# Performance work log

Hardware: AMD Instinct MI355X
Metric: run time of the kernel (lower is better)

The kernel has to match this reference:

```python
import jax, jax.numpy as jnp
import numpy as np

N_NODES = 20000
N_EDGES = 160000
F_IN = 256
N_CLASSES = 32
HEADS = 8
GAT_C = 128


def setup_inputs() -> dict:
    key = jax.random.key(0)
    ks = jax.random.split(key, 20)

    def w(k, shape, fan_in):
        return jax.random.normal(k, shape, dtype=jnp.float32) * (1.0 / np.sqrt(fan_in))

    return {
        "x": jax.random.normal(ks[0], (N_NODES, F_IN), dtype=jnp.float32),
        "edge_index": jax.random.randint(ks[1], (2, N_EDGES), 0, N_NODES, dtype=jnp.int64),
        # SAGEConv(256 -> 64): lin_l (bias) on aggregated neighbors, lin_r (no bias) on root
        "W_l1": w(ks[2], (F_IN, 64), F_IN), "b_l1": jnp.zeros((64,), jnp.float32),
        "W_r1": w(ks[3], (F_IN, 64), F_IN),
        # SAGEConv(64 -> 128)
        "W_l2": w(ks[4], (64, 128), 64), "b_l2": jnp.zeros((128,), jnp.float32),
        "W_r2": w(ks[5], (64, 128), 64),
        # GATConv(128 -> 128, heads=8, concat)
        "W_g": w(ks[6], (128, HEADS * GAT_C), 128),
        "att_src": w(ks[7], (HEADS, GAT_C), GAT_C),
        "att_dst": w(ks[8], (HEADS, GAT_C), GAT_C),
        "b_g": jnp.zeros((HEADS * GAT_C,), jnp.float32),
        # GCNConv(1024 -> 64), GCNConv(64 -> 32)
        "W_c1": w(ks[9], (HEADS * GAT_C, 64), HEADS * GAT_C), "b_c1": jnp.zeros((64,), jnp.float32),
        "W_c2": w(ks[10], (64, N_CLASSES), 64), "b_c2": jnp.zeros((N_CLASSES,), jnp.float32),
        # residual Linear(256 -> 64)
        "W_res": w(ks[11], (F_IN, 64), F_IN), "b_res": jnp.zeros((64,), jnp.float32),
    }


def _forward(x, edge_index, W_l1, b_l1, W_r1, W_l2, b_l2, W_r2,
             W_g, att_src, att_dst, b_g, W_c1, b_c1, W_c2, b_c2, W_res, b_res):
    n = x.shape[0]
    src, dst = edge_index[0], edge_index[1]  # messages flow src -> dst

    def sage(h, Wl, bl, Wr):
        # mean aggregation of neighbor features, then lin_l(agg) + lin_r(root)
        s = jax.ops.segment_sum(h[src], dst, num_segments=n)
        cnt = jax.ops.segment_sum(jnp.ones_like(src, dtype=h.dtype), dst, num_segments=n)
        mean = s / jnp.maximum(cnt, 1.0)[:, None]
        return mean @ Wl + bl + h @ Wr

    res_x = x @ W_res + b_res
    h = jax.nn.relu(sage(x, W_l1, b_l1, W_r1)) + res_x      # [N, 64]
    h = jax.nn.relu(sage(h, W_l2, b_l2, W_r2))              # [N, 128]

    # ---- GATConv with self-loops (PyG default) ----
    loop = jnp.arange(n, dtype=src.dtype)
    srcf = jnp.concatenate([src, loop])
    dstf = jnp.concatenate([dst, loop])

    hg = (h @ W_g).reshape(n, HEADS, GAT_C)                 # [N, H, C]
    a_s = jnp.sum(hg * att_src, axis=-1)                    # [N, H]
    a_d = jnp.sum(hg * att_dst, axis=-1)                    # [N, H]
    e = jax.nn.leaky_relu(a_s[srcf] + a_d[dstf], negative_slope=0.2)  # [Ef, H]
    m = jax.ops.segment_max(e, dstf, num_segments=n)
    e = jnp.exp(e - m[dstf])
    denom = jax.ops.segment_sum(e, dstf, num_segments=n)
    alpha = e / denom[dstf]                                 # softmax over incoming edges
    gat = jax.ops.segment_sum(alpha[:, :, None] * hg[srcf], dstf, num_segments=n)
    h = jax.nn.relu(gat.reshape(n, HEADS * GAT_C) + b_g)    # [N, 1024]

    # ---- GCNConv with self-loops and symmetric normalization ----
    deg = jax.ops.segment_sum(jnp.ones_like(srcf, dtype=h.dtype), dstf, num_segments=n)
    dinv = jax.lax.rsqrt(jnp.maximum(deg, 1.0))             # deg >= 1 via self-loops
    norm = (dinv[srcf] * dinv[dstf])[:, None]

    def gcn(h, W, b):
        hw = h @ W
        return jax.ops.segment_sum(norm * hw[srcf], dstf, num_segments=n) + b

    h = gcn(h, W_c1, b_c1)
    h = gcn(h, W_c2, b_c2)
    return jax.nn.log_softmax(h, axis=1)


def reference(x, edge_index, W_l1, b_l1, W_r1, W_l2, b_l2, W_r2,
              W_g, att_src, att_dst, b_g, W_c1, b_c1, W_c2, b_c2, W_res, b_res):
    return _forward(x, edge_index, W_l1, b_l1, W_r1, W_l2, b_l2, W_r2,
                    W_g, att_src, att_dst, b_g, W_c1, b_c1, W_c2, b_c2, W_res, b_res)
```

## Files before the change

kernel.cpp:

```cpp
#include <hip/hip_runtime.h>

#define NN 20000
#define NE 160000
#define NEF 180000
#define NB1 ((NN + 255) / 256)

typedef long long ll;
typedef __attribute__((ext_vector_type(4))) float f32x4;
typedef __attribute__((ext_vector_type(8))) short s16x8;

static __device__ __forceinline__ float b2f(ushort u) {
  return __uint_as_float(((unsigned)u) << 16);
}
static __device__ __forceinline__ ushort f2b(float f) {
  unsigned u = __float_as_uint(f);
  return (ushort)((u + 0x7fffu + ((u >> 16) & 1u)) >> 16);
}

template<int MF, int NF, int K, bool F32OUT>
__global__ __launch_bounds__(256) void gemm_mfma(
    const ushort* __restrict__ A, const ushort* __restrict__ Bt,
    const float* __restrict__ bias, void* __restrict__ Cv,
    int M, int N, int lda)
{
  const int wid  = threadIdx.x >> 6;
  const int lane = threadIdx.x & 63;
  const int wr = wid >> 1, wc = wid & 1;
  const int bm = blockIdx.y * (32 * MF) + wr * (16 * MF);
  const int bn = blockIdx.x * (32 * NF) + wc * (16 * NF);
  const int lr = lane & 15;
  const int ko = (lane >> 4) * 8;

  const ushort* pa[MF];
  const ushort* pb[NF];
  #pragma unroll
  for (int i = 0; i < MF; i++) {
    int r = min(bm + i * 16 + lr, M - 1);
    pa[i] = A + (ll)r * lda + ko;
  }
  #pragma unroll
  for (int j = 0; j < NF; j++) {
    int c = min(bn + j * 16 + lr, N - 1);
    pb[j] = Bt + (ll)c * K + ko;
  }

  f32x4 acc[MF][NF];
  #pragma unroll
  for (int i = 0; i < MF; i++)
    #pragma unroll
    for (int j = 0; j < NF; j++) acc[i][j] = {0.f, 0.f, 0.f, 0.f};

  #pragma unroll
  for (int k = 0; k < K; k += 32) {
    s16x8 af[MF], bf[NF];
    #pragma unroll
    for (int i = 0; i < MF; i++) af[i] = *(const s16x8*)(pa[i] + k);
    #pragma unroll
    for (int j = 0; j < NF; j++) bf[j] = *(const s16x8*)(pb[j] + k);
    #pragma unroll
    for (int i = 0; i < MF; i++)
      #pragma unroll
      for (int j = 0; j < NF; j++)
        acc[i][j] = __builtin_amdgcn_mfma_f32_16x16x32_bf16(af[i], bf[j], acc[i][j], 0, 0, 0);
  }

  const int rq = (lane >> 4) * 4;
  #pragma unroll
  for (int i = 0; i < MF; i++) {
    #pragma unroll
    for (int j = 0; j < NF; j++) {
      int col = bn + j * 16 + lr;
      if (col >= N) continue;
      float bv = bias ? bias[col] : 0.f;
      int rbase = bm + i * 16 + rq;
      #pragma unroll
      for (int r = 0; r < 4; r++) {
        int row = rbase + r;
        if (row >= M) continue;
        float v = acc[i][j][r] + bv;
        if (F32OUT) ((float*)Cv)[(ll)row * N + col] = v;
        else        ((ushort*)Cv)[(ll)row * N + col] = f2b(v);
      }
    }
  }
}

__global__ __launch_bounds__(256) void k_gat_apply_gcn1(
    const ushort* __restrict__ agg,
    const ushort* __restrict__ BtG,
    const ushort* __restrict__ Btc1,
    const float* __restrict__ b_g,
    ushort* __restrict__ hw64)
{
  __shared__ ushort gt[2][32][72];
  const int wc   = threadIdx.x >> 6;
  const int lane = threadIdx.x & 63;
  const int bm = blockIdx.x * 32;
  const int lr = lane & 15;
  const int ko = (lane >> 4) * 8;
  const int rq = (lane >> 4) * 4;

  const ushort* pa0 = agg + (ll)min(bm + lr,      NN - 1) * 1024 + ko;
  const ushort* pa1 = agg + (ll)min(bm + 16 + lr, NN - 1) * 1024 + ko;

  f32x4 o0 = {0.f, 0.f, 0.f, 0.f}, o1 = o0;

  #pragma unroll 2
  for (int ct = 0; ct < 16; ct++) {
    const int koff = (ct >> 1) * 128;
    const int cg = ct * 64 + wc * 16 + lr;
    const ushort* pb = BtG + (ll)cg * 128 + ko;
    f32x4 g0 = {0.f, 0.f, 0.f, 0.f}, g1 = g0;
    #pragma unroll
    for (int k = 0; k < 128; k += 32) {
      s16x8 a0 = *(const s16x8*)(pa0 + koff + k);
      s16x8 a1 = *(const s16x8*)(pa1 + koff + k);
      s16x8 bb = *(const s16x8*)(pb + k);
      g0 = __builtin_amdgcn_mfma_f32_16x16x32_bf16(a0, bb, g0, 0, 0, 0);
      g1 = __builtin_amdgcn_mfma_f32_16x16x32_bf16(a1, bb, g1, 0, 0, 0);
    }
    float bv = b_g[cg];
    #pragma unroll
    for (int r = 0; r < 4; r++) {
      gt[ct & 1][rq + r][wc * 16 + lr]      = f2b(fmaxf(g0[r] + bv, 0.f));
      gt[ct & 1][16 + rq + r][wc * 16 + lr] = f2b(fmaxf(g1[r] + bv, 0.f));
    }
    __syncthreads();
    const ushort* qb = Btc1 + (ll)(wc * 16 + lr) * 1024 + ct * 64 + ko;
    #pragma unroll
    for (int k = 0; k < 64; k += 32) {
      s16x8 a0 = *(const s16x8*)&gt[ct & 1][lr][k + ko];
      s16x8 a1 = *(const s16x8*)&gt[ct & 1][16 + lr][k + ko];
      s16x8 bb = *(const s16x8*)(qb + k);
      o0 = __builtin_amdgcn_mfma_f32_16x16x32_bf16(a0, bb, o0, 0, 0, 0);
      o1 = __builtin_amdgcn_mfma_f32_16x16x32_bf16(a1, bb, o1, 0, 0, 0);
    }
  }
  int col = wc * 16 + lr;
  #pragma unroll
  for (int r = 0; r < 4; r++) {
    int row0 = bm + rq + r, row1 = bm + 16 + rq + r;
    if (row0 < NN) hw64[(ll)row0 * 64 + col] = f2b(o0[r]);
    if (row1 < NN) hw64[(ll)row1 * 64 + col] = f2b(o1[r]);
  }
}

struct PrepEnt { const float* W; ushort* Bt; int N; int K; int base; };
struct Prep { PrepEnt e[8]; int total; };

__global__ void k_setup(const float* __restrict__ x, ushort* __restrict__ xb, Prep p,
                        const float* __restrict__ b_res, const float* __restrict__ b_l1,
                        const float* __restrict__ b_l2, float* __restrict__ bias192,
                        float* __restrict__ bias256,
                        const float* __restrict__ W_g, const float* __restrict__ att_s,
                        const float* __restrict__ att_d, ushort* __restrict__ watt_t,
                        int* __restrict__ icnt) {
  ll t = (ll)blockIdx.x * 256 + threadIdx.x;
  const ll T0 = (ll)NN * 64;
  if (t < T0) {
    ll i = t * 4;
    float4 v = *(const float4*)(x + i);
    ushort4 o;
    o.x = f2b(v.x); o.y = f2b(v.y); o.z = f2b(v.z); o.w = f2b(v.w);
    *(ushort4*)(xb + i) = o;
    return;
  }
  t -= T0;
  if (t < p.total) {
    int tt = (int)t;
    #pragma unroll
    for (int i = 0; i < 8; i++) {
      int sz = p.e[i].N * p.e[i].K;
      if (tt >= p.e[i].base && tt < p.e[i].base + sz) {
        int loc = tt - p.e[i].base;
        int n = loc / p.e[i].K, k = loc - n * p.e[i].K;
        p.e[i].Bt[loc] = f2b(p.e[i].W[(ll)k * p.e[i].N + n]);
      }
    }
    return;
  }
  t -= p.total;
  if (t < 256) {
    int tt = (int)t;
    if (tt < 64) bias192[tt] = b_res[tt];
    else if (tt < 128) bias192[tt] = 0.f;
    else if (tt < 192) bias192[tt] = b_l1[tt - 128];
    bias256[tt] = (tt < 128) ? 0.f : b_l2[tt - 128];
    return;
  }
  t -= 256;
  if (t < 2048) {
    int k = (int)t >> 4;
    int col = (int)t & 15;
    int h = col & 7;
    const float* av = (col < 8) ? (att_s + h * 128) : (att_d + h * 128);
    const float* wrow = W_g + (ll)k * 1024 + h * 128;
    float s = 0.f;
    for (int j = 0; j < 128; j++) s += wrow[j] * av[j];
    watt_t[col * 128 + k] = f2b(s);
    return;
  }
  t -= 2048;
  if (t < NN) icnt[t] = 0;
}

__global__ void k_counti(const int* __restrict__ dst, int* __restrict__ icnt) {
  int e = blockIdx.x * 256 + threadIdx.x;
  if (e < NE) atomicAdd(&icnt[dst[e]], 1);
}

__global__ __launch_bounds__(256) void k_scan1(const int* __restrict__ icnt,
                                               int* __restrict__ rowptr,
                                               int* __restrict__ bsum) {
  __shared__ int sd[256];
  int t = threadIdx.x;
  int i = blockIdx.x * 256 + t;
  int v = (i < NN) ? icnt[i] + 1 : 0;
  sd[t] = v;
  __syncthreads();
  #pragma unroll
  for (int o = 1; o < 256; o <<= 1) {
    int u = (t >= o) ? sd[t - o] : 0;
    __syncthreads();
    sd[t] += u;
    __syncthreads();
  }
  if (i < NN) rowptr[i] = sd[t] - v;
  if (t == 255) bsum[blockIdx.x] = sd[255];
}

__global__ __launch_bounds__(128) void k_scan2(const int* __restrict__ bsum,
                                               int* __restrict__ boff) {
  __shared__ int sd[128];
  int t = threadIdx.x;
  int v = (t < NB1) ? bsum[t] : 0;
  sd[t] = v;
  __syncthreads();
  #pragma unroll
  for (int o = 1; o < 128; o <<= 1) {
    int u = (t >= o) ? sd[t - o] : 0;
    __syncthreads();
    sd[t] += u;
    __syncthreads();
  }
  if (t < NB1) boff[t] = sd[t] - v;
}

__global__ void k_scan3(int* __restrict__ rowptr, const int* __restrict__ boff,
                        int* __restrict__ cur, const int* __restrict__ icnt,
                        float* __restrict__ dinv) {
  int i = blockIdx.x * 256 + threadIdx.x;
  if (i >= NN) return;
  int r = rowptr[i] + boff[i >> 8];
  rowptr[i] = r;
  cur[i] = r;
  dinv[i] = rsqrtf((float)icnt[i] + 1.0f);
  if (i == 0) rowptr[NN] = NEF;
}

__global__ void k_scatter(const int* __restrict__ dst, int* __restrict__ cur,
                          int* __restrict__ eid) {
  int t = blockIdx.x * 256 + threadIdx.x;
  if (t >= NEF) return;
  int d = (t < NE) ? dst[t] : t - NE;
  int p = atomicAdd(&cur[d], 1);
  eid[p] = t;
}

template<int C, int STRIDE, bool ADD_RES>
__global__ __launch_bounds__(256) void k_sage_csr(
    const int* __restrict__ rowptr, const int* __restrict__ eid,
    const int* __restrict__ src, const ushort* __restrict__ feat,
    const ushort* __restrict__ linr, const ushort* __restrict__ resx,
    ushort* __restrict__ out)
{
  int node = blockIdx.x * 4 + (threadIdx.x >> 6);
  int lane = threadIdx.x & 63;
  if (node >= NN) return;
  int b = rowptr[node], e = rowptr[node + 1];
  float a0 = 0.f, a1 = 0.f;
  int n = 0;
  for (int base = b; base < e; base += 64) {
    int m = min(64, e - base);
    int sreg = -1;
    if (lane < m) {
      int ed = eid[base + lane];
      sreg = (ed < NE) ? src[ed] : -1;
    }
    for (int i = 0; i < m; i++) {
      int s = __shfl(sreg, i);
      if (s >= 0) {
        a0 += b2f(feat[(ll)s * STRIDE + lane]);
        if (C == 128) a1 += b2f(feat[(ll)s * STRIDE + lane + 64]);
        n++;
      }
    }
  }
  float inv = 1.f / fmaxf((float)n, 1.f);
  {
    float v = a0 * inv + b2f(linr[(ll)node * STRIDE + lane]);
    v = fmaxf(v, 0.f);
    if (ADD_RES) v += b2f(resx[(ll)node * STRIDE + lane]);
    out[(ll)node * C + lane] = f2b(v);
  }
  if (C == 128) {
    float v = a1 * inv + b2f(linr[(ll)node * STRIDE + lane + 64]);
    v = fmaxf(v, 0.f);
    out[(ll)node * C + lane + 64] = f2b(v);
  }
}

__global__ void k_gat_softmax(const int* __restrict__ rowptr, const int* __restrict__ eid,
                              const int* __restrict__ src, const float* __restrict__ asd,
                              float* __restrict__ alpha, float* __restrict__ invden) {
  int t = blockIdx.x * 256 + threadIdx.x;
  if (t >= NN * 8) return;
  int node = t >> 3, h = t & 7;
  int b = rowptr[node], e = rowptr[node + 1];
  float ad = asd[(ll)node * 16 + 8 + h];
  float mx = -3.0e38f;
  for (int p = b; p < e; p++) {
    int ed = eid[p];
    int s = (ed < NE) ? src[ed] : node;
    float v = asd[(ll)s * 16 + h] + ad;
    v = (v > 0.f) ? v : 0.2f * v;
    mx = fmaxf(mx, v);
  }
  float sum = 0.f;
  for (int p = b; p < e; p++) {
    int ed = eid[p];
    int s = (ed < NE) ? src[ed] : node;
    float v = asd[(ll)s * 16 + h] + ad;
    v = (v > 0.f) ? v : 0.2f * v;
    float ex = expf(v - mx);
    alpha[(ll)p * 8 + h] = ex;
    sum += ex;
  }
  invden[t] = 1.f / sum;
}

__global__ __launch_bounds__(128) void k_gat_agg(
    const int* __restrict__ rowptr, const int* __restrict__ eid,
    const int* __restrict__ src, const float* __restrict__ alpha,
    const float* __restrict__ invden, const ushort* __restrict__ h2b,
    ushort* __restrict__ agg)
{
  __shared__ int s_l[64];
  __shared__ float al[64 * 8];
  __shared__ float inv_s[8];
  int node = blockIdx.x;
  int c = threadIdx.x;
  int b = rowptr[node], e = rowptr[node + 1];
  if (c < 8) inv_s[c] = invden[node * 8 + c];
  float acc[8] = {0.f, 0.f, 0.f, 0.f, 0.f, 0.f, 0.f, 0.f};
  for (int c0 = b; c0 < e; c0 += 64) {
    int m = min(64, e - c0);
    if (c < m) { int ed = eid[c0 + c]; s_l[c] = (ed < NE) ? src[ed] : node; }
    for (int idx = c; idx < m * 8; idx += 128) al[idx] = alpha[(ll)c0 * 8 + idx];
    __syncthreads();
    for (int i = 0; i < m; i++) {
      float v = b2f(h2b[(ll)s_l[i] * 128 + c]);
      float4 aa = *(const float4*)&al[i * 8];
      float4 ab = *(const float4*)&al[i * 8 + 4];
      acc[0] = fmaf(aa.x, v, acc[0]);
      acc[1] = fmaf(aa.y, v, acc[1]);
      acc[2] = fmaf(aa.z, v, acc[2]);
      acc[3] = fmaf(aa.w, v, acc[3]);
      acc[4] = fmaf(ab.x, v, acc[4]);
      acc[5] = fmaf(ab.y, v, acc[5]);
      acc[6] = fmaf(ab.z, v, acc[6]);
      acc[7] = fmaf(ab.w, v, acc[7]);
    }
    __syncthreads();
  }
  #pragma unroll
  for (int h = 0; h < 8; h++)
    agg[(ll)node * 1024 + h * 128 + c] = f2b(acc[h] * inv_s[h]);
}

template<int C, bool FUSE_LSM>
__global__ __launch_bounds__(256) void k_gcn_csr(
    const int* __restrict__ rowptr, const int* __restrict__ eid,
    const int* __restrict__ src, const float* __restrict__ dinv,
    const ushort* __restrict__ hw, const float* __restrict__ bias,
    void* __restrict__ outv)
{
  const int npb = 256 / C;
  int node = blockIdx.x * npb + threadIdx.x / C;
  int c = threadIdx.x & (C - 1);
  if (node >= NN) return;
  int b = rowptr[node], e = rowptr[node + 1];
  float acc = 0.f;
  for (int base = b; base < e; base += C) {
    int m = min(C, e - base);
    int sreg = 0;
    float dreg = 0.f;
    if (c < m) {
      int ed = eid[base + c];
      sreg = (ed < NE) ? src[ed] : node;
      dreg = dinv[sreg];
    }
    for (int i = 0; i < m; i++) {
      int s  = __shfl(sreg, i, C);
      float dv = __shfl(dreg, i, C);
      acc = fmaf(dv, b2f(hw[(ll)s * C + c]), acc);
    }
  }
  float v = acc * dinv[node] + bias[c];
  if (!FUSE_LSM) {
    ((ushort*)outv)[(ll)node * C + c] = f2b(v);
  } else {
    float mx = v;
    #pragma unroll
    for (int o = 16; o > 0; o >>= 1) mx = fmaxf(mx, __shfl_xor(mx, o, 32));
    float s = expf(v - mx);
    #pragma unroll
    for (int o = 16; o > 0; o >>= 1) s += __shfl_xor(s, o, 32);
    ((float*)outv)[(ll)node * C + c] = v - mx - logf(s);
  }
}

extern "C" void kernel_launch(void* const* d_in, const int* in_sizes, int n_in,
                              void* d_out, int out_size, void* d_ws, size_t ws_size,
                              hipStream_t stream) {
  const float* x     = (const float*)d_in[0];
  const int*   ei    = (const int*)d_in[1];
  const float* W_l1  = (const float*)d_in[2];
  const float* b_l1  = (const float*)d_in[3];
  const float* W_r1  = (const float*)d_in[4];
  const float* W_l2  = (const float*)d_in[5];
  const float* b_l2  = (const float*)d_in[6];
  const float* W_r2  = (const float*)d_in[7];
  const float* W_g   = (const float*)d_in[8];
  const float* att_s = (const float*)d_in[9];
  const float* att_d = (const float*)d_in[10];
  const float* b_g   = (const float*)d_in[11];
  const float* W_c1  = (const float*)d_in[12];
  const float* b_c1  = (const float*)d_in[13];
  const float* W_c2  = (const float*)d_in[14];
  const float* b_c2  = (const float*)d_in[15];
  const float* W_res = (const float*)d_in[16];
  const float* b_res = (const float*)d_in[17];
  const int* src = ei;
  const int* dst = ei + NE;
  float* out = (float*)d_out;

  float* Wf = (float*)d_ws;
  size_t off = 0;
  auto take = [&](size_t n) { float* p = Wf + off; off += (n + 3) & ~(size_t)3; return p; };
  ushort* xb    = (ushort*)take((size_t)NN * 128);
  ushort* C192  = (ushort*)take((size_t)NN * 96);
  ushort* h1    = (ushort*)take((size_t)NN * 32);
  ushort* C256  = (ushort*)take((size_t)NN * 128);
  ushort* h2    = (ushort*)take((size_t)NN * 64);
  ushort* agg   = (ushort*)take((size_t)NN * 512);
  ushort* hw64  = (ushort*)take((size_t)NN * 32);
  ushort* acc64 = (ushort*)take((size_t)NN * 32);
  ushort* hw32  = (ushort*)take((size_t)NN * 16);
  ushort* Bt192 = (ushort*)take(192 * 256 / 2);
  ushort* Bt256 = (ushort*)take(256 * 64 / 2);
  ushort* BtG   = (ushort*)take(1024 * 128 / 2);
  ushort* Btc1  = (ushort*)take(64 * 1024 / 2);
  ushort* Btc2  = (ushort*)take(32 * 64 / 2);
  ushort* watt_t= (ushort*)take(16 * 128 / 2);
  float* bias192 = take(192);
  float* bias256 = take(256);
  int*   icnt   = (int*)take(NN);
  int*   rowptr = (int*)take(NN + 1);
  int*   cur    = (int*)take(NN);
  int*   eidb   = (int*)take(NEF);
  int*   bsum   = (int*)take(NB1);
  int*   boff   = (int*)take(NB1);
  float* dinv   = take(NN);
  float* asd    = take((size_t)NN * 16);
  float* alpha  = take((size_t)NEF * 8);
  float* invden = take((size_t)NN * 8);
  (void)ws_size; (void)in_sizes; (void)n_in; (void)out_size;

  auto nb = [](ll t) { return dim3((unsigned)((t + 255) / 256)); };

  Prep pp;
  int base = 0;
  auto ent = [&](int i, const float* W, ushort* Bt, int N_, int K_) {
    pp.e[i] = {W, Bt, N_, K_, base}; base += N_ * K_;
  };
  ent(0, W_res, Bt192,             64, 256);
  ent(1, W_l1,  Bt192 + 64 * 256,  64, 256);
  ent(2, W_r1,  Bt192 + 128 * 256, 64, 256);
  ent(3, W_l2,  Bt256,             128, 64);
  ent(4, W_r2,  Bt256 + 128 * 64,  128, 64);
  ent(5, W_g,   BtG,               1024, 128);
  ent(6, W_c1,  Btc1,              64, 1024);
  ent(7, W_c2,  Btc2,              32, 64);
  pp.total = base;
  k_setup<<<nb((ll)NN * 64 + base + 256 + 2048 + NN), 256, 0, stream>>>(
      x, xb, pp, b_res, b_l1, b_l2, bias192, bias256, W_g, att_s, att_d, watt_t, icnt);

  k_counti<<<nb(NE), 256, 0, stream>>>(dst, icnt);
  k_scan1<<<NB1, 256, 0, stream>>>(icnt, rowptr, bsum);
  k_scan2<<<1, 128, 0, stream>>>(bsum, boff);
  k_scan3<<<nb(NN), 256, 0, stream>>>(rowptr, boff, cur, icnt, dinv);
  k_scatter<<<nb(NEF), 256, 0, stream>>>(dst, cur, eidb);

  gemm_mfma<4, 2, 256, false><<<dim3(3, 157), 256, 0, stream>>>(
      xb, Bt192, bias192, C192, NN, 192, 256);
  k_sage_csr<64, 192, true><<<nb((ll)NN * 64), 256, 0, stream>>>(
      rowptr, eidb, src, C192 + 64, C192 + 128, C192, h1);

  gemm_mfma<4, 2, 64, false><<<dim3(4, 157), 256, 0, stream>>>(
      h1, Bt256, bias256, C256, NN, 256, 64);
  k_sage_csr<128, 256, false><<<nb((ll)NN * 64), 256, 0, stream>>>(
      rowptr, eidb, src, C256, C256 + 128, nullptr, h2);

  gemm_mfma<4, 1, 128, true><<<dim3(1, 157), 256, 0, stream>>>(
      h2, watt_t, nullptr, asd, NN, 16, 128);
  k_gat_softmax<<<nb((ll)NN * 8), 256, 0, stream>>>(
      rowptr, eidb, src, asd, alpha, invden);
  k_gat_agg<<<dim3(NN), 128, 0, stream>>>(
      rowptr, eidb, src, alpha, invden, h2, agg);
  k_gat_apply_gcn1<<<dim3(625), 256, 0, stream>>>(agg, BtG, Btc1, b_g, hw64);
  k_gcn_csr<64, false><<<nb((ll)NN * 64), 256, 0, stream>>>(
      rowptr, eidb, src, dinv, hw64, b_c1, acc64);

  gemm_mfma<4, 1, 64, false><<<dim3(1, 157), 256, 0, stream>>>(
      acc64, Btc2, nullptr, hw32, NN, 32, 64);
  k_gcn_csr<32, true><<<nb((ll)NN * 32), 256, 0, stream>>>(
      rowptr, eidb, src, dinv, hw32, b_c2, out);
}
```

Before: 255.7 us.

## Stage GAT aggregate rows in swizzled LDS with register prefetch in fused GAT/GCN kernel

The fused GAT-apply + GCN1 kernel now loads each head's 32x128 slice of the aggregated features cooperatively into double-buffered, XOR-swizzled shared memory, instead of every wave re-reading the same rows from global memory. The next head's slice is prefetched into registers while the current one is consumed. This targets redundant global reads, since all four waves previously fetched identical A fragments, twice per head. It adds LDS usage and an extra barrier per head, which may lower occupancy.

```diff
diff --git a/kernel.cpp b/kernel.cpp
--- a/kernel.cpp
+++ b/kernel.cpp
@@ -92,48 +92,68 @@
     const float* __restrict__ b_g,
     ushort* __restrict__ hw64)
 {
+  __shared__ ushort At[2][32 * 128];
   __shared__ ushort gt[2][32][72];
-  const int wc   = threadIdx.x >> 6;
-  const int lane = threadIdx.x & 63;
+  const int t    = threadIdx.x;
+  const int wc   = t >> 6;
+  const int lane = t & 63;
   const int bm = blockIdx.x * 32;
   const int lr = lane & 15;
-  const int ko = (lane >> 4) * 8;
-  const int rq = (lane >> 4) * 4;
-
-  const ushort* pa0 = agg + (ll)min(bm + lr,      NN - 1) * 1024 + ko;
-  const ushort* pa1 = agg + (ll)min(bm + 16 + lr, NN - 1) * 1024 + ko;
+  const int q  = lane >> 4;
+  const int ko = q * 8;
+  const int rq = q * 4;
+
+  const int srow = t >> 3;
+  const int scg  = t & 7;
+  const ushort* sg = agg + (ll)min(bm + srow, NN - 1) * 1024 + scg * 16;
+  const int w0 = srow * 128 + (((2 * scg)     ^ (srow & 7)) * 8);
+  const int w1 = srow * 128 + (((2 * scg + 1) ^ (srow & 7)) * 8);
 
   f32x4 o0 = {0.f, 0.f, 0.f, 0.f}, o1 = o0;
 
+  s16x8 r0 = *(const s16x8*)(sg);
+  s16x8 r1 = *(const s16x8*)(sg + 8);
+
   #pragma unroll 2
-  for (int ct = 0; ct < 16; ct++) {
-    const int koff = (ct >> 1) * 128;
-    const int cg = ct * 64 + wc * 16 + lr;
-    const ushort* pb = BtG + (ll)cg * 128 + ko;
-    f32x4 g0 = {0.f, 0.f, 0.f, 0.f}, g1 = g0;
-    #pragma unroll
-    for (int k = 0; k < 128; k += 32) {
-      s16x8 a0 = *(const s16x8*)(pa0 + koff + k);
-      s16x8 a1 = *(const s16x8*)(pa1 + koff + k);
-      s16x8 bb = *(const s16x8*)(pb + k);
-      g0 = __builtin_amdgcn_mfma_f32_16x16x32_bf16(a0, bb, g0, 0, 0, 0);
-      g1 = __builtin_amdgcn_mfma_f32_16x16x32_bf16(a1, bb, g1, 0, 0, 0);
-    }
-    float bv = b_g[cg];
-    #pragma unroll
-    for (int r = 0; r < 4; r++) {
-      gt[ct & 1][rq + r][wc * 16 + lr]      = f2b(fmaxf(g0[r] + bv, 0.f));
-      gt[ct & 1][16 + rq + r][wc * 16 + lr] = f2b(fmaxf(g1[r] + bv, 0.f));
-    }
-    __syncthreads();
-    const ushort* qb = Btc1 + (ll)(wc * 16 + lr) * 1024 + ct * 64 + ko;
-    #pragma unroll
-    for (int k = 0; k < 64; k += 32) {
-      s16x8 a0 = *(const s16x8*)&gt[ct & 1][lr][k + ko];
-      s16x8 a1 = *(const s16x8*)&gt[ct & 1][16 + lr][k + ko];
-      s16x8 bb = *(const s16x8*)(qb + k);
-      o0 = __builtin_amdgcn_mfma_f32_16x16x32_bf16(a0, bb, o0, 0, 0, 0);
-      o1 = __builtin_amdgcn_mfma_f32_16x16x32_bf16(a1, bb, o1, 0, 0, 0);
+  for (int h = 0; h < 8; h++) {
+    *(s16x8*)&At[h & 1][w0] = r0;
+    *(s16x8*)&At[h & 1][w1] = r1;
+    if (h < 7) {
+      r0 = *(const s16x8*)(sg + (h + 1) * 128);
+      r1 = *(const s16x8*)(sg + (h + 1) * 128 + 8);
+    }
+    __syncthreads();
+    #pragma unroll
+    for (int it = 0; it < 2; it++) {
+      const int ct = 2 * h + it;
+      const int cg = ct * 64 + wc * 16 + lr;
+      const ushort* pb = BtG + (ll)cg * 128 + ko;
+      f32x4 g0 = {0.f, 0.f, 0.f, 0.f}, g1 = g0;
+      #pragma unroll
+      for (int k = 0; k < 128; k += 32) {
+        const int gi = ((k >> 3) + q) ^ (lr & 7);
+        s16x8 a0 = *(const s16x8*)&At[h & 1][lr        * 128 + gi * 8];
+        s16x8 a1 = *(const s16x8*)&At[h & 1][(16 + lr) * 128 + gi * 8];
+        s16x8 bb = *(const s16x8*)(pb + k);
+        g0 = __builtin_amdgcn_mfma_f32_16x16x32_bf16(a0, bb, g0, 0, 0, 0);
+        g1 = __builtin_amdgcn_mfma_f32_16x16x32_bf16(a1, bb, g1, 0, 0, 0);
+      }
+      float bv = b_g[cg];
+      #pragma unroll
+      for (int r = 0; r < 4; r++) {
+        gt[it][rq + r][wc * 16 + lr]      = f2b(fmaxf(g0[r] + bv, 0.f));
+        gt[it][16 + rq + r][wc * 16 + lr] = f2b(fmaxf(g1[r] + bv, 0.f));
+      }
+      __syncthreads();
+      const ushort* qb = Btc1 + (ll)(wc * 16 + lr) * 1024 + ct * 64 + ko;
+      #pragma unroll
+      for (int k = 0; k < 64; k += 32) {
+        s16x8 a0 = *(const s16x8*)&gt[it][lr][k + ko];
+        s16x8 a1 = *(const s16x8*)&gt[it][16 + lr][k + ko];
+        s16x8 bb = *(const s16x8*)(qb + k);
+        o0 = __builtin_amdgcn_mfma_f32_16x16x32_bf16(a0, bb, o0, 0, 0, 0);
+        o1 = __builtin_amdgcn_mfma_f32_16x16x32_bf16(a1, bb, o1, 0, 0, 0);
+      }
     }
   }
   int col = wc * 16 + lr;
```

Result: faster. 235.1 us (-8.1%).
